# Optimization experiments

Measured on AMD Instinct MI355X. Metric: run time of the kernel, lower is better.

## Reference

```python
import jax, jax.numpy as jnp
import numpy as np

TEMPERATURE = 1.0
# softmax over 32768 db entries gives mean score ~3e-5; threshold 5e-5 makes the
# mask non-trivial (torch default threshold=0.0 would keep everything).
THRESHOLD = 5e-5


def setup_inputs() -> dict:
    key = jax.random.key(0)
    kq, kd = jax.random.split(key)
    queries = jax.random.normal(kq, (8192, 512), dtype=jnp.float32)
    db = jax.random.normal(kd, (32768, 512), dtype=jnp.float32)
    return {"queries": queries, "db": db, "k": 20}


def reference(queries, db, k):
    # similarity matmul: [Nq, Ndb]
    sim_mat = (queries @ db.T) / TEMPERATURE
    # torch does .float().softmax(dim=1)
    all_scores = jax.nn.softmax(sim_mat.astype(jnp.float32), axis=1)
    # db is provided explicitly -> mask_diag = False; k = min(k, db_size)
    k = min(k, db.shape[0])
    topk_scores, topk_inds = jax.lax.top_k(all_scores, k)  # sorted=True
    mask = topk_scores > THRESHOLD
    n_retrieved_per_query = mask.sum(axis=1)
    # padded equivalent of the nonzero-gather: below-threshold slots zeroed
    retrieved_scores = jnp.where(mask, topk_scores, 0.0)
    return retrieved_scores, topk_inds, n_retrieved_per_query, mask
```

## Files before the change

kernel.cpp:

```cpp
#include <hip/hip_runtime.h>
#include <hip/hip_bf16.h>
#include <float.h>
#include <limits.h>

#define NQ 8192
#define ND 32768
#define KD 512
#define TOPK 20
#define NCAND 32
#define NS 16
#define SLICE 2048
#define SEMIT 24
#define EBASE 64.0f

typedef _Float16 f16x8 __attribute__((ext_vector_type(8)));
typedef _Float16 f16x4 __attribute__((ext_vector_type(4)));
typedef float    f32x4 __attribute__((ext_vector_type(4)));

#define CSW(a, b) { unsigned mx_ = (a) > (b) ? (a) : (b); \
                    unsigned mn_ = (a) > (b) ? (b) : (a); (a) = mx_; (b) = mn_; }

__global__ __launch_bounds__(256) void tohalf(
    const float* __restrict__ src, _Float16* __restrict__ dst, int n4)
{
  int g = blockIdx.x * 256 + threadIdx.x;
  if (g >= n4) return;
  float4 v = ((const float4*)src)[g];
  f16x4 h = {(_Float16)v.x, (_Float16)v.y, (_Float16)v.z, (_Float16)v.w};
  ((f16x4*)dst)[g] = h;
}

__device__ __forceinline__ void gload16(const _Float16* g, _Float16* l) {
  __builtin_amdgcn_global_load_lds(
      (const __attribute__((address_space(1))) unsigned int*)g,
      (__attribute__((address_space(3))) unsigned int*)l, 16, 0, 0);
}

__global__ __launch_bounds__(256, 2) void fusedsel(
    const _Float16* __restrict__ Qh, const _Float16* __restrict__ Dh,
    unsigned* __restrict__ scand, float* __restrict__ ssum)
{
  __shared__ _Float16 Bs[128 * 64];

  const int t = threadIdx.x;
  const int w = t >> 6, l = t & 63;
  const int m0 = blockIdx.x * 64;
  const int ns = blockIdx.y;
  const int lane_mn = l & 15, quad = l >> 4;
  const int myrow = m0 + w * 16 + lane_mn;

  f16x8 af[16];
  #pragma unroll
  for (int i = 0; i < 16; i++)
    af[i] = *(const f16x8*)(Qh + (size_t)myrow * KD + i * 32 + quad * 8);

  const int sRowIn = l >> 3;
  const int sq = (l & 7) ^ (sRowIn & 7);
  const int fs0 = quad ^ (lane_mn & 7);
  const int fs1 = fs0 ^ 4;

  unsigned L0=0,L1=0,L2=0,L3=0,L4=0,L5=0,L6=0,L7=0;
  float es = 0.f;

  for (int ni = 0; ni < SLICE / 128; ni++) {
    const int n0 = ns * SLICE + ni * 128;
    f32x4 acc[8];
    #pragma unroll
    for (int i = 0; i < 8; i++) acc[i] = (f32x4){0.f, 0.f, 0.f, 0.f};

    #pragma unroll
    for (int kk = 0; kk < 8; kk++) {
      __syncthreads();
      #pragma unroll
      for (int j = 0; j < 4; j++)
        gload16(Dh + (size_t)(n0 + w * 8 + j * 32 + sRowIn) * KD + kk * 64 + sq * 8,
                Bs + (w * 8 + j * 32) * 64);
      __syncthreads();

      #pragma unroll
      for (int jj = 0; jj < 2; jj++) {
        const int fs = jj ? fs1 : fs0;
        #pragma unroll
        for (int mt = 0; mt < 8; mt++) {
          f16x8 db = *(const f16x8*)&Bs[(mt * 16 + lane_mn) * 64 + fs * 8];
          acc[mt] = __builtin_amdgcn_mfma_f32_16x16x32_f16(
              db, af[2 * kk + jj], acc[mt], 0, 0, 0);
        }
      }
    }

    #pragma unroll
    for (int mt = 0; mt < 8; mt++) {
      #pragma unroll
      for (int reg = 0; reg < 4; reg++) {
        float v = acc[mt][reg];
        _Float16 h = (_Float16)v;
        float vq = (float)h;
        es += __expf(vq - EBASE);
        unsigned short b = __builtin_bit_cast(unsigned short, h);
        unsigned u = (unsigned)b ^ 0x8000u ^
                     ((unsigned)(-(int)(b >> 15)) & 0x7FFFu);
        unsigned key = (u << 16) |
                       (unsigned)(0x7FFF - (n0 + mt * 16 + quad * 4 + reg));
        if (key > L7) {
          L7 = key;
          CSW(L6, L7); CSW(L5, L6); CSW(L4, L5); CSW(L3, L4);
          CSW(L2, L3); CSW(L1, L2); CSW(L0, L1);
        }
      }
    }
  }

  es += __shfl_xor(es, 16);
  es += __shfl_xor(es, 32);
  if (quad == 0) ssum[(size_t)myrow * NS + ns] = es;

  for (int s = 0; s < SEMIT; s++) {
    unsigned bk = L0;
    unsigned o = __shfl_xor(bk, 16); bk = bk > o ? bk : o;
    o = __shfl_xor(bk, 32);          bk = bk > o ? bk : o;
    if (L0 == bk) { L0=L1; L1=L2; L2=L3; L3=L4; L4=L5; L5=L6; L6=L7; L7=0; }
    if (quad == 0) scand[(size_t)myrow * (NS * SEMIT) + ns * SEMIT + s] = bk;
  }
}

__global__ __launch_bounds__(256) void mergecand(
    const unsigned* __restrict__ scand, const float* __restrict__ ssum,
    float* __restrict__ cand_aval, int* __restrict__ cand_idx,
    float* __restrict__ mz)
{
  const int row = blockIdx.x * 4 + (threadIdx.x >> 6);
  const int l = threadIdx.x & 63;
  const unsigned* rk = scand + (size_t)row * (NS * SEMIT);

  unsigned M0=0,M1=0,M2=0,M3=0,M4=0,M5=0;
  #pragma unroll
  for (int j = 0; j < 6; j++) {
    unsigned k = rk[l * 6 + j];
    if (k > M5) {
      M5 = k;
      CSW(M4, M5); CSW(M3, M4); CSW(M2, M3); CSW(M1, M2); CSW(M0, M1);
    }
  }

  float za = (l < NS) ? ssum[(size_t)row * NS + l] : 0.f;
  #pragma unroll
  for (int off = 32; off > 0; off >>= 1) za += __shfl_xor(za, off);

  for (int s = 0; s < NCAND; s++) {
    unsigned bk = M0;
    #pragma unroll
    for (int off = 32; off > 0; off >>= 1) {
      unsigned o = __shfl_xor(bk, off); bk = bk > o ? bk : o;
    }
    if (M0 == bk) { M0=M1; M1=M2; M2=M3; M3=M4; M4=M5; M5=0; }
    if (l == 0) {
      unsigned u = bk >> 16;
      unsigned bs = (u >= 0x8000u) ? (u ^ 0x8000u) : (u ^ 0xFFFFu);
      _Float16 hv = __builtin_bit_cast(_Float16, (unsigned short)bs);
      cand_aval[(size_t)row * NCAND + s] = (float)hv;
      cand_idx [(size_t)row * NCAND + s] = 0x7FFF - (int)(bk & 0x7FFFu);
    }
  }
  if (l == 0) {
    mz[(size_t)row * 2 + 0] = EBASE;
    mz[(size_t)row * 2 + 1] = za;
  }
}

__global__ __launch_bounds__(256) void rescore(
    const float* __restrict__ Q, const float* __restrict__ DB,
    const int* __restrict__ cand_idx, float* __restrict__ exact)
{
  __shared__ float dbS[256][65];
  __shared__ float qS[8][64];
  __shared__ int idxS[256];
  const int t = threadIdx.x;
  const int row0g = blockIdx.x * 8;
  idxS[t] = cand_idx[(size_t)row0g * NCAND + t];
  const int myrow = t >> 5;
  const int sc4 = t >> 2;
  const int sf = t & 3;
  float acc = 0.f;

  for (int k0 = 0; k0 < KD; k0 += 64) {
    __syncthreads();
    #pragma unroll
    for (int cb = 0; cb < 4; cb++) {
      int c = cb * 64 + sc4;
      const float* dp = DB + (size_t)idxS[c] * KD + k0 + sf * 4;
      #pragma unroll
      for (int j = 0; j < 4; j++) {
        float4 v = *(const float4*)(dp + j * 16);
        int e = sf * 4 + j * 16;
        dbS[c][e] = v.x; dbS[c][e + 1] = v.y;
        dbS[c][e + 2] = v.z; dbS[c][e + 3] = v.w;
      }
    }
    if (t < 128) {
      int qr = t >> 4, fi = t & 15;
      float4 v = *(const float4*)(Q + (size_t)(row0g + qr) * KD + k0 + fi * 4);
      *(float4*)&qS[qr][fi * 4] = v;
    }
    __syncthreads();
    #pragma unroll 8
    for (int e = 0; e < 64; e++)
      acc = fmaf(qS[myrow][e], dbS[t][e], acc);
  }
  exact[(size_t)row0g * NCAND + t] = acc;
}

__global__ __launch_bounds__(256) void finalize(
    const float* __restrict__ exact, const float* __restrict__ cand_aval,
    const int* __restrict__ cand_idx, const float* __restrict__ mz,
    float* __restrict__ out)
{
  const int row = blockIdx.x * 4 + (threadIdx.x >> 6);
  const int l = threadIdx.x & 63;
  const bool real = (l < NCAND);

  float e  = real ? exact[(size_t)row * NCAND + l] : -FLT_MAX;
  float av = real ? cand_aval[(size_t)row * NCAND + l] : -FLT_MAX;
  int  idx = real ? cand_idx[(size_t)row * NCAND + l] : INT_MAX;
  const float Ma = mz[(size_t)row * 2 + 0];
  const float Za = mz[(size_t)row * 2 + 1];

  float Me = e;
  #pragma unroll
  for (int off = 32; off > 0; off >>= 1) Me = fmaxf(Me, __shfl_xor(Me, off));

  float ce = real ? __expf(e - Me) : 0.f;
  float ca = real ? __expf(av - Ma) : 0.f;
  float Se = ce, Sa = ca;
  #pragma unroll
  for (int off = 32; off > 0; off >>= 1) {
    Se += __shfl_xor(Se, off);
    Sa += __shfl_xor(Sa, off);
  }
  float Ta = Za - Sa; if (Ta < 0.f) Ta = 0.f;
  const float Ze = Se + Ta * __expf(Ma - Me);

  int rank = 0;
  for (int j = 0; j < NCAND; j++) {
    float ej = __shfl(e, j);
    int   ij = __shfl(idx, j);
    rank += ((ej > e) || (ej == e && ij < idx)) ? 1 : 0;
  }

  const size_t oS = 0;
  const size_t oI = (size_t)NQ * TOPK;
  const size_t oN = (size_t)2 * NQ * TOPK;
  const size_t oM = (size_t)2 * NQ * TOPK + NQ;

  const bool write = real && (rank < TOPK);
  float sc = ce / Ze;
  bool msk = write && ((double)sc > 5e-5);
  if (write) {
    out[oS + (size_t)row * TOPK + rank] = msk ? sc : 0.f;
    out[oI + (size_t)row * TOPK + rank] = (float)idx;
    out[oM + (size_t)row * TOPK + rank] = msk ? 1.f : 0.f;
  }
  unsigned long long bal = __ballot(msk);
  if (l == 0) out[oN + row] = (float)__popcll(bal);
}

extern "C" void kernel_launch(void* const* d_in, const int* in_sizes, int n_in,
                              void* d_out, int out_size, void* d_ws, size_t ws_size,
                              hipStream_t stream) {
  const float* queries = (const float*)d_in[0];
  const float* db      = (const float*)d_in[1];
  float* out = (float*)d_out;

  char* base = (char*)d_ws;
  unsigned* scandP = (unsigned*)base;
  float* ssumP = (float*)(scandP + (size_t)NQ * NS * SEMIT);
  float* exactP = ssumP + (size_t)NQ * NS;
  float* avalP  = exactP + (size_t)NQ * NCAND;
  int*   idxP   = (int*)(avalP + (size_t)NQ * NCAND);
  float* mzP    = (float*)(idxP + (size_t)NQ * NCAND);
  _Float16* Qh  = (_Float16*)(mzP + (size_t)NQ * 2);
  _Float16* Dh  = Qh + (size_t)NQ * KD;

  const int n4q = NQ * KD / 4, n4d = ND * KD / 4;
  tohalf<<<n4q / 256, 256, 0, stream>>>(queries, Qh, n4q);
  tohalf<<<n4d / 256, 256, 0, stream>>>(db, Dh, n4d);

  fusedsel<<<dim3(NQ / 64, NS), 256, 0, stream>>>(Qh, Dh, scandP, ssumP);
  mergecand<<<NQ / 4, 256, 0, stream>>>(scandP, ssumP, avalP, idxP, mzP);
  rescore<<<NQ / 8, 256, 0, stream>>>(queries, db, idxP, exactP);
  finalize<<<NQ / 4, 256, 0, stream>>>(exactP, avalP, idxP, mzP, out);
}
```

Before: 601.6 us.

## Double query rows per warp to reuse LDS tiles; pack fp16 epilogue conversions

Each warp now holds two 16-row query fragments and issues two MFMAs per shared db fragment, so the block covers 128 query rows and each db tile loaded into LDS serves twice as many rows. This halves the global-to-LDS traffic per unit of compute. The epilogue converts accumulator pairs with a packed round-toward-zero fp16 conversion, builds the sort keys two at a time, and uses a raw exp2 with a fused scale. It roughly doubles register use for A fragments, accumulators and the per-row top-8 lists, which risks occupancy and spills under the two-waves launch bound. The rounding mode also changes from nearest to toward-zero, which can perturb candidate ordering.

After: 577.8 us. 1.04x faster.

```diff
diff --git a/kernel.cpp b/kernel.cpp
--- a/kernel.cpp
+++ b/kernel.cpp
@@ -15,10 +15,16 @@
 
 typedef _Float16 f16x8 __attribute__((ext_vector_type(8)));
 typedef _Float16 f16x4 __attribute__((ext_vector_type(4)));
+typedef __fp16   hp16x2 __attribute__((ext_vector_type(2)));
 typedef float    f32x4 __attribute__((ext_vector_type(4)));
 
 #define CSW(a, b) { unsigned mx_ = (a) > (b) ? (a) : (b); \
                     unsigned mn_ = (a) > (b) ? (b) : (a); (a) = mx_; (b) = mn_; }
+
+__device__ __forceinline__ float fexp64(float q) {
+  return __builtin_amdgcn_exp2f(__builtin_fmaf(q, 1.44269504f,
+                                               -EBASE * 1.44269504f));
+}
 
 __global__ __launch_bounds__(256) void tohalf(
     const float* __restrict__ src, _Float16* __restrict__ dst, int n4)
@@ -36,6 +42,24 @@
       (__attribute__((address_space(3))) unsigned int*)l, 16, 0, 0);
 }
 
+#define INSL(x) if ((x) > L7) { L7 = (x); \
+  CSW(L6, L7); CSW(L5, L6); CSW(L4, L5); CSW(L3, L4); \
+  CSW(L2, L3); CSW(L1, L2); CSW(L0, L1); }
+#define INSM(x) if ((x) > M7) { M7 = (x); \
+  CSW(M6, M7); CSW(M5, M6); CSW(M4, M5); CSW(M3, M4); \
+  CSW(M2, M3); CSW(M1, M2); CSW(M0, M1); }
+
+#define EPIPAIR(va, vb, c0, ES, INS) { \
+  hp16x2 hp_ = __builtin_amdgcn_cvt_pkrtz((va), (vb)); \
+  unsigned pk_ = __builtin_bit_cast(unsigned, hp_); \
+  ES += fexp64((float)hp_[0]); \
+  ES += fexp64((float)hp_[1]); \
+  unsigned sg_ = (pk_ >> 15) & 0x10001u; \
+  unsigned u2_ = pk_ ^ (0x80008000u ^ (sg_ * 0x7FFFu)); \
+  unsigned k0_ = (u2_ << 16) | (unsigned)(c0); \
+  unsigned k1_ = (u2_ & 0xFFFF0000u) | (unsigned)((c0) - 1); \
+  INS(k0_); INS(k1_); }
+
 __global__ __launch_bounds__(256, 2) void fusedsel(
     const _Float16* __restrict__ Qh, const _Float16* __restrict__ Dh,
     unsigned* __restrict__ scand, float* __restrict__ ssum)
@@ -44,15 +68,18 @@
 
   const int t = threadIdx.x;
   const int w = t >> 6, l = t & 63;
-  const int m0 = blockIdx.x * 64;
+  const int m0 = blockIdx.x * 128;
   const int ns = blockIdx.y;
   const int lane_mn = l & 15, quad = l >> 4;
-  const int myrow = m0 + w * 16 + lane_mn;
-
-  f16x8 af[16];
-  #pragma unroll
-  for (int i = 0; i < 16; i++)
-    af[i] = *(const f16x8*)(Qh + (size_t)myrow * KD + i * 32 + quad * 8);
+  const int row0 = m0 + w * 32 + lane_mn;
+  const int row1 = row0 + 16;
+
+  f16x8 af0[16], af1[16];
+  #pragma unroll
+  for (int i = 0; i < 16; i++) {
+    af0[i] = *(const f16x8*)(Qh + (size_t)row0 * KD + i * 32 + quad * 8);
+    af1[i] = *(const f16x8*)(Qh + (size_t)row1 * KD + i * 32 + quad * 8);
+  }
 
   const int sRowIn = l >> 3;
   const int sq = (l & 7) ^ (sRowIn & 7);
@@ -60,13 +87,17 @@
   const int fs1 = fs0 ^ 4;
 
   unsigned L0=0,L1=0,L2=0,L3=0,L4=0,L5=0,L6=0,L7=0;
-  float es = 0.f;
+  unsigned M0=0,M1=0,M2=0,M3=0,M4=0,M5=0,M6=0,M7=0;
+  float es0 = 0.f, es1 = 0.f;
 
   for (int ni = 0; ni < SLICE / 128; ni++) {
     const int n0 = ns * SLICE + ni * 128;
-    f32x4 acc[8];
-    #pragma unroll
-    for (int i = 0; i < 8; i++) acc[i] = (f32x4){0.f, 0.f, 0.f, 0.f};
+    f32x4 acc0[8], acc1[8];
+    #pragma unroll
+    for (int i = 0; i < 8; i++) {
+      acc0[i] = (f32x4){0.f, 0.f, 0.f, 0.f};
+      acc1[i] = (f32x4){0.f, 0.f, 0.f, 0.f};
+    }
 
     #pragma unroll
     for (int kk = 0; kk < 8; kk++) {
@@ -83,44 +114,45 @@
         #pragma unroll
         for (int mt = 0; mt < 8; mt++) {
           f16x8 db = *(const f16x8*)&Bs[(mt * 16 + lane_mn) * 64 + fs * 8];
-          acc[mt] = __builtin_amdgcn_mfma_f32_16x16x32_f16(
-              db, af[2 * kk + jj], acc[mt], 0, 0, 0);
+          acc0[mt] = __builtin_amdgcn_mfma_f32_16x16x32_f16(
+              db, af0[2 * kk + jj], acc0[mt], 0, 0, 0);
+          acc1[mt] = __builtin_amdgcn_mfma_f32_16x16x32_f16(
+              db, af1[2 * kk + jj], acc1[mt], 0, 0, 0);
         }
       }
     }
 
+    const int cb = 0x7FFF - n0 - quad * 4;
     #pragma unroll
     for (int mt = 0; mt < 8; mt++) {
-      #pragma unroll
-      for (int reg = 0; reg < 4; reg++) {
-        float v = acc[mt][reg];
-        _Float16 h = (_Float16)v;
-        float vq = (float)h;
-        es += __expf(vq - EBASE);
-        unsigned short b = __builtin_bit_cast(unsigned short, h);
-        unsigned u = (unsigned)b ^ 0x8000u ^
-                     ((unsigned)(-(int)(b >> 15)) & 0x7FFFu);
-        unsigned key = (u << 16) |
-                       (unsigned)(0x7FFF - (n0 + mt * 16 + quad * 4 + reg));
-        if (key > L7) {
-          L7 = key;
-          CSW(L6, L7); CSW(L5, L6); CSW(L4, L5); CSW(L3, L4);
-          CSW(L2, L3); CSW(L1, L2); CSW(L0, L1);
-        }
-      }
-    }
-  }
-
-  es += __shfl_xor(es, 16);
-  es += __shfl_xor(es, 32);
-  if (quad == 0) ssum[(size_t)myrow * NS + ns] = es;
+      const int c0 = cb - mt * 16;
+      EPIPAIR(acc0[mt][0], acc0[mt][1], c0,     es0, INSL);
+      EPIPAIR(acc0[mt][2], acc0[mt][3], c0 - 2, es0, INSL);
+      EPIPAIR(acc1[mt][0], acc1[mt][1], c0,     es1, INSM);
+      EPIPAIR(acc1[mt][2], acc1[mt][3], c0 - 2, es1, INSM);
+    }
+  }
+
+  es0 += __shfl_xor(es0, 16); es0 += __shfl_xor(es0, 32);
+  es1 += __shfl_xor(es1, 16); es1 += __shfl_xor(es1, 32);
+  if (quad == 0) {
+    ssum[(size_t)row0 * NS + ns] = es0;
+    ssum[(size_t)row1 * NS + ns] = es1;
+  }
 
   for (int s = 0; s < SEMIT; s++) {
     unsigned bk = L0;
     unsigned o = __shfl_xor(bk, 16); bk = bk > o ? bk : o;
     o = __shfl_xor(bk, 32);          bk = bk > o ? bk : o;
     if (L0 == bk) { L0=L1; L1=L2; L2=L3; L3=L4; L4=L5; L5=L6; L6=L7; L7=0; }
-    if (quad == 0) scand[(size_t)myrow * (NS * SEMIT) + ns * SEMIT + s] = bk;
+    if (quad == 0) scand[(size_t)row0 * (NS * SEMIT) + ns * SEMIT + s] = bk;
+  }
+  for (int s = 0; s < SEMIT; s++) {
+    unsigned bk = M0;
+    unsigned o = __shfl_xor(bk, 16); bk = bk > o ? bk : o;
+    o = __shfl_xor(bk, 32);          bk = bk > o ? bk : o;
+    if (M0 == bk) { M0=M1; M1=M2; M2=M3; M3=M4; M4=M5; M5=M6; M6=M7; M7=0; }
+    if (quad == 0) scand[(size_t)row1 * (NS * SEMIT) + ns * SEMIT + s] = bk;
   }
 }
 
@@ -285,7 +317,7 @@
   tohalf<<<n4q / 256, 256, 0, stream>>>(queries, Qh, n4q);
   tohalf<<<n4d / 256, 256, 0, stream>>>(db, Dh, n4d);
 
-  fusedsel<<<dim3(NQ / 64, NS), 256, 0, stream>>>(Qh, Dh, scandP, ssumP);
+  fusedsel<<<dim3(NQ / 128, NS), 256, 0, stream>>>(Qh, Dh, scandP, ssumP);
   mergecand<<<NQ / 4, 256, 0, stream>>>(scandP, ssumP, avalP, idxP, mzP);
   rescore<<<NQ / 8, 256, 0, stream>>>(queries, db, idxP, exactP);
   finalize<<<NQ / 4, 256, 0, stream>>>(exactP, avalP, idxP, mzP, out);
```
